# Optimization experiments

Measured on AMD Instinct MI355X. Metric: run time of the kernel, lower is better.

Reference implementation:

```python
import math
import jax, jax.numpy as jnp
import numpy as np

C = 256          # channels
HID = 64         # max(int(C*0.25),16)
RH = 64          # max(C//4,32) router hidden
N, S, H, W = 8, 64, 16, 16
LOW_FREQ_RATIO = 0.2
ROUTER_TEMP = 1.0
LN_EPS = 1e-5

def gelu(v):
    return jax.nn.gelu(v, approximate=False)

def bn1d(v, s, b):  # folded eval-mode BatchNorm1d: (N,C,S)
    return v * s[None, :, None] + b[None, :, None]

def conv1x1(v, w, b=None):  # v:(N,Cin,S), w:(Cout,Cin)
    o = jnp.einsum('oc,ncs->nos', w, v)
    if b is not None:
        o = o + b[None, :, None]
    return o

def convk(v, w):  # v:(N,Cin,S), w:(Cout,Cin,K), 'same' padding
    k = w.shape[-1]
    return jax.lax.conv_general_dilated(v, w, (1,), [(k // 2, k // 2)],
                                        dimension_numbers=('NCH', 'OIH', 'NCH'))

def setup_inputs():
    key = jax.random.key(0)
    ks = iter(jax.random.split(key, 64))
    def nrm(shape, sc=0.02):
        return jax.random.normal(next(ks), shape, jnp.float32) * sc
    d = {}
    d['x'] = jax.random.normal(next(ks), (N, C, S, H, W), jnp.float32)
    d['ln_g'] = jnp.ones((C,), jnp.float32)
    d['ln_b'] = jnp.zeros((C,), jnp.float32)
    for k in (3, 5, 7):
        d['mb_w%d' % k] = nrm((C, 3 * C, k))
        d['mb_s%d' % k] = 1.0 + nrm((C,))
        d['mb_b%d' % k] = nrm((C,))
    d['mf_w'] = nrm((C, C)); d['mf_s'] = 1.0 + nrm((C,)); d['mf_b'] = nrm((C,))
    d['pg_w1'] = nrm((HID, 3)); d['pg_s1'] = 1.0 + nrm((HID,)); d['pg_b1'] = nrm((HID,))
    d['pg_w2'] = nrm((C, HID)); d['pg_b2'] = nrm((C,))
    d['pp_w'] = nrm((C, C)); d['pp_s'] = 1.0 + nrm((C,)); d['pp_b'] = nrm((C,))
    d['mg_w'] = nrm((C, 2 * C)); d['mg_b'] = nrm((C,))
    d['mo_w1'] = nrm((C, 3 * C)); d['mo_s1'] = 1.0 + nrm((C,)); d['mo_b1'] = nrm((C,))
    d['mo_w2'] = nrm((C, C))
    d['rt_w1'] = nrm((RH, C + 5)); d['rt_b1'] = nrm((RH,))
    d['rt_w2'] = nrm((3, RH)); d['rt_b2'] = nrm((3,))
    d['bp_w1'] = nrm((C, 4 * C)); d['bp_s1'] = 1.0 + nrm((C,)); d['bp_b1'] = nrm((C,))
    d['bp_w2'] = nrm((C, C))
    d['res_scale'] = jnp.full((1, C, 1), 0.05, jnp.float32)
    d['fg_w'] = nrm((C, C)); d['fg_b'] = nrm((C,))
    d['sg_w'] = nrm((C, C)); d['sg_s'] = 1.0 + nrm((C,)); d['sg_b'] = nrm((C,))
    return d

def _forward(x, ln_g, ln_b, mb_w3, mb_s3, mb_b3, mb_w5, mb_s5, mb_b5,
             mb_w7, mb_s7, mb_b7, mf_w, mf_s, mf_b,
             pg_w1, pg_s1, pg_b1, pg_w2, pg_b2, pp_w, pp_s, pp_b,
             mg_w, mg_b, mo_w1, mo_s1, mo_b1, mo_w2,
             rt_w1, rt_b1, rt_w2, rt_b2, bp_w1, bp_s1, bp_b1, bp_w2,
             res_scale, fg_w, fg_b, sg_w, sg_s, sg_b):
    n, c, s = x.shape[:3]
    x32 = x.astype(jnp.float32)
    desc = x32.mean(axis=(-1, -2))                     # (N,C,S)
    t = desc.transpose(0, 2, 1)                        # (N,S,C)
    mu = t.mean(-1, keepdims=True)
    var = t.var(-1, keepdims=True)
    dn = (((t - mu) / jnp.sqrt(var + LN_EPS)) * ln_g + ln_b).transpose(0, 2, 1)  # (N,C,S)

    def tdiff(v, order):
        dd = v[:, :, order:] - v[:, :, :-order]
        return jnp.pad(dd, ((0, 0), (0, 0), (order, 0)))
    diff1 = tdiff(dn, 1)
    diff2 = tdiff(dn, 2)

    # motion branch (multi-kernel conv1d + BN + GELU)
    mi = jnp.concatenate([dn, diff1, diff2], axis=1)   # (N,3C,S)
    motion = 0.0
    for w, bs, bb in ((mb_w3, mb_s3, mb_b3), (mb_w5, mb_s5, mb_b5), (mb_w7, mb_s7, mb_b7)):
        motion = motion + gelu(bn1d(convk(mi, w), bs, bb))
    motion = gelu(bn1d(conv1x1(motion / 3.0, mf_w), mf_s, mf_b))

    # FFT-based cycle / phase estimation
    tokens = dn.transpose(0, 2, 1)                     # (N,S,C)
    freq = jnp.fft.rfft(tokens, axis=1, norm='ortho')  # (N,F,C) complex
    fe = jnp.abs(freq).mean(-1)                        # (N,F)
    Fb = fe.shape[1]
    low = min(max(int(round(Fb * LOW_FREQ_RATIO)), 1), Fb - 1)
    he = fe[:, low:]
    peak_rel = jnp.argmax(he, axis=-1)                 # (N,)
    peak_idx = peak_rel + low
    peak_val = jnp.take_along_axis(he, peak_rel[:, None], axis=1)
    cycle_conf = peak_val / jnp.maximum(he.sum(axis=1, keepdims=True), 1e-6)  # (N,1)
    peak_norm = peak_idx.astype(jnp.float32)[:, None] / float(Fb - 1)
    mean_freq = freq.mean(-1)                          # (N,F) complex
    dom = jnp.take_along_axis(mean_freq, peak_idx[:, None], axis=1)[:, 0]
    dom_phase = jnp.arctan2(dom.imag, dom.real)
    tax = jnp.arange(s, dtype=jnp.float32)
    ang = (2.0 * math.pi / max(s, 1)) * peak_idx.astype(jnp.float32)
    arg = ang[:, None] * tax[None, :] + dom_phase[:, None]
    phase_cos = jnp.cos(arg)[:, None, :]               # (N,1,S)
    phase_sin = jnp.sin(arg)[:, None, :]

    cycle_token = jnp.broadcast_to(cycle_conf[:, :, None], (n, 1, s))
    pf = jnp.concatenate([phase_cos, phase_sin, cycle_token], axis=1)  # (N,3,S)
    pgate = jax.nn.sigmoid(conv1x1(gelu(bn1d(conv1x1(pf, pg_w1), pg_s1, pg_b1)), pg_w2, pg_b2))
    phase = gelu(bn1d(conv1x1(dn * pgate, pp_w), pp_s, pp_b))

    # bidirectional EMA memory via lax.scan
    gate = jax.nn.sigmoid(conv1x1(jnp.concatenate([dn, jnp.abs(diff1)], axis=1), mg_w, mg_b))
    g = gate.transpose(2, 0, 1)                        # (S,N,C)
    dd = dn.transpose(2, 0, 1)
    def step(st, gd):
        gt, dt = gd
        st = gt * st + (1.0 - gt) * dt
        return st, st
    _, fo = jax.lax.scan(step, dd[0], (g[1:], dd[1:]))
    fwd_mem = jnp.concatenate([dd[:1], fo], axis=0).transpose(1, 2, 0)
    _, bo = jax.lax.scan(step, dd[-1], (g[-2::-1], dd[-2::-1]))
    bwd_mem = jnp.concatenate([dd[-1:], bo], axis=0)[::-1].transpose(1, 2, 0)
    memory = conv1x1(gelu(bn1d(conv1x1(
        jnp.concatenate([dn, fwd_mem, bwd_mem], axis=1), mo_w1), mo_s1, mo_b1)), mo_w2)

    # router
    seq_std = dn.std(axis=2).mean(axis=1, keepdims=True)
    diff_energy = jnp.abs(diff1).mean(axis=(1, 2))[:, None]
    motion_energy = jnp.abs(motion).mean(axis=(1, 2))[:, None]
    memory_energy = jnp.abs(memory - dn).mean(axis=(1, 2))[:, None]
    stats = jnp.concatenate([seq_std, diff_energy, cycle_conf, peak_norm,
                             memory_energy + motion_energy], axis=-1)
    ri = jnp.concatenate([dn.mean(-1), stats], axis=-1)  # (N,C+5)
    hdn = gelu(ri @ rt_w1.T + rt_b1)
    logits = hdn @ rt_w2.T + rt_b2
    bw = jax.nn.softmax(logits / max(ROUTER_TEMP, 1e-6), axis=-1)  # (N,3)
    fused = (bw[:, 0, None, None] * motion + bw[:, 1, None, None] * phase
             + bw[:, 2, None, None] * memory)

    delta = conv1x1(gelu(bn1d(conv1x1(
        jnp.concatenate([dn, fused, motion - phase, memory - dn], axis=1),
        bp_w1), bp_s1, bp_b1)), bp_w2)
    delta = delta * jax.nn.sigmoid(conv1x1(dn, fg_w, fg_b))
    delta = res_scale * delta
    delta = delta[:, :, :, None, None]                 # (N,C,S,1,1)

    sp = x32.mean(axis=2)                              # (N,C,H,W)
    sg_lin = jnp.einsum('oc,nchw->nohw', sg_w, sp)
    sgate = jax.nn.sigmoid(sg_lin * sg_s[None, :, None, None] + sg_b[None, :, None, None])
    delta = delta * sgate[:, :, None, :, :]            # (N,C,S,H,W)
    return x + delta.astype(x.dtype)

def reference(x, ln_g, ln_b, mb_w3, mb_s3, mb_b3, mb_w5, mb_s5, mb_b5,
              mb_w7, mb_s7, mb_b7, mf_w, mf_s, mf_b,
              pg_w1, pg_s1, pg_b1, pg_w2, pg_b2, pp_w, pp_s, pp_b,
              mg_w, mg_b, mo_w1, mo_s1, mo_b1, mo_w2,
              rt_w1, rt_b1, rt_w2, rt_b2, bp_w1, bp_s1, bp_b1, bp_w2,
              res_scale, fg_w, fg_b, sg_w, sg_s, sg_b):
    return _forward(x, ln_g, ln_b, mb_w3, mb_s3, mb_b3, mb_w5, mb_s5, mb_b5,
                    mb_w7, mb_s7, mb_b7, mf_w, mf_s, mf_b,
                    pg_w1, pg_s1, pg_b1, pg_w2, pg_b2, pp_w, pp_s, pp_b,
                    mg_w, mg_b, mo_w1, mo_s1, mo_b1, mo_w2,
                    rt_w1, rt_b1, rt_w2, rt_b2, bp_w1, bp_s1, bp_b1, bp_w2,
                    res_scale, fg_w, fg_b, sg_w, sg_s, sg_b)
```

## Files before the change

### kernel.cpp

```cpp
#include <hip/hip_runtime.h>
#include <math.h>

namespace {

constexpr int N_ = 8, C_ = 256, S_ = 64, HW_ = 256;
constexpr int NS = N_ * S_;
constexpr int NHW = N_ * HW_;

constexpr size_t O_DESC  = 0;
constexpr size_t O_DN    = 131072;
constexpr size_t O_MSUM  = 262144;
constexpr size_t O_MOT   = 393216;
constexpr size_t O_GATE  = 524288;
constexpr size_t O_HMO   = 655360;
constexpr size_t O_MEM   = 786432;
constexpr size_t O_PPIN  = 917504;
constexpr size_t O_PHASE = 1048576;
constexpr size_t O_FGATE = 1179648;
constexpr size_t O_HBP   = 1310720;
constexpr size_t O_DELTA = 1441792;
constexpr size_t O_GIB   = 1572864;
constexpr size_t O_MOI   = 1835008;
constexpr size_t O_BPI   = 2228224;
constexpr size_t O_SPT   = 2752512;
constexpr size_t O_SGATE = 3276800;
constexpr size_t O_FE    = 3801088;
constexpr size_t O_MFRE  = 3801600;
constexpr size_t O_MFIM  = 3802112;
constexpr size_t O_PK    = 3802624;
constexpr size_t O_BW    = 3802656;
constexpr size_t O_ATMF  = 3802688;
constexpr size_t O_ATMG  = 3868224;
constexpr size_t O_ATMO1 = 3999296;
constexpr size_t O_ATMO2 = 4195904;
constexpr size_t O_ATPP  = 4261440;
constexpr size_t O_ATBP1 = 4326976;
constexpr size_t O_ATBP2 = 4589120;
constexpr size_t O_ATFG  = 4654656;
constexpr size_t O_ATSG  = 4720192;
constexpr size_t O_WFRAG = 4785728;
constexpr size_t O_IM2   = 6850112;
constexpr size_t O_CONVC = 8226368;

typedef __attribute__((ext_vector_type(4))) float f32x4;
typedef __attribute__((ext_vector_type(8))) short s16x8;
typedef __attribute__((ext_vector_type(8))) unsigned short u16x8;

__device__ __forceinline__ float gelu_f(float v) {
  return 0.5f * v * (1.0f + erff(v * 0.70710678118654752f));
}
__device__ __forceinline__ float sigmoid_f(float v) {
  return 1.0f / (1.0f + expf(-v));
}
__device__ __forceinline__ unsigned short f2bf(float f) {
  unsigned int u = __float_as_uint(f);
  u += 0x7fffu + ((u >> 16) & 1u);
  return (unsigned short)(u >> 16);
}

__device__ __forceinline__ float block_sum256(float v, float* scratch) {
  #pragma unroll
  for (int off = 32; off; off >>= 1) v += __shfl_down(v, off, 64);
  int w = threadIdx.x >> 6;
  __syncthreads();
  if ((threadIdx.x & 63) == 0) scratch[w] = v;
  __syncthreads();
  return scratch[0] + scratch[1] + scratch[2] + scratch[3];
}

__global__ __launch_bounds__(256) void transpose_kernel(
    const float* __restrict__ wmf, const float* __restrict__ wmg,
    const float* __restrict__ wmo1, const float* __restrict__ wmo2,
    const float* __restrict__ wpp, const float* __restrict__ wbp1,
    const float* __restrict__ wbp2, const float* __restrict__ wfg,
    const float* __restrict__ wsg, float* __restrict__ ws) {
  __shared__ float tile[32][33];
  int xt = blockIdx.x, yt = blockIdx.y;
  const float* src; float* dst; int K;
  if      (xt < 8)   { src = wmf;  dst = ws + O_ATMF;  K = 256;  }
  else if (xt < 24)  { src = wmg;  dst = ws + O_ATMG;  K = 512;  xt -= 8;  }
  else if (xt < 48)  { src = wmo1; dst = ws + O_ATMO1; K = 768;  xt -= 24; }
  else if (xt < 56)  { src = wmo2; dst = ws + O_ATMO2; K = 256;  xt -= 48; }
  else if (xt < 64)  { src = wpp;  dst = ws + O_ATPP;  K = 256;  xt -= 56; }
  else if (xt < 96)  { src = wbp1; dst = ws + O_ATBP1; K = 1024; xt -= 64; }
  else if (xt < 104) { src = wbp2; dst = ws + O_ATBP2; K = 256;  xt -= 96; }
  else if (xt < 112) { src = wfg;  dst = ws + O_ATFG;  K = 256;  xt -= 104;}
  else               { src = wsg;  dst = ws + O_ATSG;  K = 256;  xt -= 112;}
  int tx = threadIdx.x & 31, ty = threadIdx.x >> 5;
  int c = xt * 32 + tx;
  #pragma unroll
  for (int i = 0; i < 4; ++i) {
    int r = yt * 32 + ty + i * 8;
    tile[ty + i * 8][tx] = src[(size_t)r * K + c];
  }
  __syncthreads();
  #pragma unroll
  for (int i = 0; i < 4; ++i) {
    int cc = xt * 32 + ty + i * 8;
    dst[(size_t)cc * 256 + yt * 32 + tx] = tile[tx][ty + i * 8];
  }
}

__global__ __launch_bounds__(256) void wfrag_kernel(
    const float* __restrict__ w3, const float* __restrict__ w5, const float* __restrict__ w7,
    unsigned short* __restrict__ wf) {
  int g = blockIdx.x * 256 + threadIdx.x;
  int lane = g & 63;
  int m16 = (g >> 6) % 48;
  int kchunk = (g >> 6) / 48;
  int o = m16 * 16 + (lane & 15);
  int conv = o >> 8, oc = o & 255;
  int q = lane >> 4;
  u16x8 out;
  #pragma unroll
  for (int j = 0; j < 8; ++j) {
    int k = kchunk * 32 + q * 8 + j;
    int ic = k / 7;
    int tau = k - ic * 7 - 3;
    float v = 0.f;
    if (conv == 0) {
      if (tau >= -1 && tau <= 1) v = w3[((size_t)oc * 768 + ic) * 3 + (tau + 1)];
    } else if (conv == 1) {
      if (tau >= -2 && tau <= 2) v = w5[((size_t)oc * 768 + ic) * 5 + (tau + 2)];
    } else {
      v = w7[((size_t)oc * 768 + ic) * 7 + (tau + 3)];
    }
    out[j] = f2bf(v);
  }
  *((u16x8*)wf + g) = out;
}

__global__ __launch_bounds__(256) void im2col_kernel(
    const float* __restrict__ dn_t, unsigned short* __restrict__ imf) {
  int g = blockIdx.x * 256 + threadIdx.x;
  int lane = g & 63;
  int c16 = (g >> 6) % 32;
  int kchunk = (g >> 6) / 32;
  int col = c16 * 16 + (lane & 15);
  int n = col >> 6, s = col & 63;
  int q = lane >> 4;
  const float* base = dn_t + (size_t)n * 16384;
  u16x8 out;
  #pragma unroll
  for (int j = 0; j < 8; ++j) {
    int k = kchunk * 32 + q * 8 + j;
    int ic = k / 7;
    int tau = k - ic * 7 - 3;
    int stream = ic >> 8, c = ic & 255;
    int sp = s + tau;
    float v = 0.f;
    if (sp >= 0 && sp < 64) {
      float d = base[(size_t)sp * 256 + c];
      if (stream == 0) v = d;
      else if (stream == 1) v = (sp >= 1) ? d - base[(size_t)(sp - 1) * 256 + c] : 0.f;
      else v = (sp >= 2) ? d - base[(size_t)(sp - 2) * 256 + c] : 0.f;
    }
    out[j] = f2bf(v);
  }
  *((u16x8*)imf + g) = out;
}

__global__ __launch_bounds__(256) void conv_mfma_kernel(
    const unsigned short* __restrict__ wf, const unsigned short* __restrict__ imf,
    float* __restrict__ partial) {
  int mt = blockIdx.x, nt = blockIdx.y, kp = blockIdx.z;
  int lane = threadIdx.x & 63;
  int w = threadIdx.x >> 6;
  int m16 = mt * 4 + w;
  const s16x8* wfp = (const s16x8*)wf;
  const s16x8* imp = (const s16x8*)imf;
  f32x4 acc0 = {0.f,0.f,0.f,0.f}, acc1 = {0.f,0.f,0.f,0.f};
  f32x4 acc2 = {0.f,0.f,0.f,0.f}, acc3 = {0.f,0.f,0.f,0.f};
  #pragma unroll 2
  for (int cc = 0; cc < 42; ++cc) {
    int kc = kp * 42 + cc;
    s16x8 a = wfp[(size_t)(kc * 48 + m16) * 64 + lane];
    s16x8 b0 = imp[(size_t)(kc * 32 + nt * 4 + 0) * 64 + lane];
    s16x8 b1 = imp[(size_t)(kc * 32 + nt * 4 + 1) * 64 + lane];
    s16x8 b2 = imp[(size_t)(kc * 32 + nt * 4 + 2) * 64 + lane];
    s16x8 b3 = imp[(size_t)(kc * 32 + nt * 4 + 3) * 64 + lane];
    acc0 = __builtin_amdgcn_mfma_f32_16x16x32_bf16(a, b0, acc0, 0, 0, 0);
    acc1 = __builtin_amdgcn_mfma_f32_16x16x32_bf16(a, b1, acc1, 0, 0, 0);
    acc2 = __builtin_amdgcn_mfma_f32_16x16x32_bf16(a, b2, acc2, 0, 0, 0);
    acc3 = __builtin_amdgcn_mfma_f32_16x16x32_bf16(a, b3, acc3, 0, 0, 0);
  }
  int q = lane >> 4, ln = lane & 15;
  int o0 = m16 * 16 + q * 4;
  float* pb = partial + (size_t)kp * 393216;
  #pragma unroll
  for (int r = 0; r < 4; ++r) {
    size_t row = (size_t)(o0 + r) * 512;
    pb[row + (nt * 4 + 0) * 16 + ln] = acc0[r];
    pb[row + (nt * 4 + 1) * 16 + ln] = acc1[r];
    pb[row + (nt * 4 + 2) * 16 + ln] = acc2[r];
    pb[row + (nt * 4 + 3) * 16 + ln] = acc3[r];
  }
}

__global__ __launch_bounds__(256) void combine_kernel(
    const float* __restrict__ P,
    const float* __restrict__ s3, const float* __restrict__ b3,
    const float* __restrict__ s5, const float* __restrict__ b5,
    const float* __restrict__ s7, const float* __restrict__ b7,
    float* __restrict__ msum) {
  __shared__ float tile[32][33];
  int col0 = blockIdx.x * 32, o0 = blockIdx.y * 32;
  int t = threadIdx.x;
  int cl = t & 31, orow = t >> 5;
  #pragma unroll
  for (int p = 0; p < 4; ++p) {
    int ol = p * 8 + orow;
    int o = o0 + ol, col = col0 + cl;
    float v3 = 0.f, v5 = 0.f, v7 = 0.f;
    #pragma unroll
    for (int kpp = 0; kpp < 4; ++kpp) {
      size_t base = (size_t)kpp * 393216 + col;
      v3 += P[base + (size_t)o * 512];
      v5 += P[base + (size_t)(o + 256) * 512];
      v7 += P[base + (size_t)(o + 512) * 512];
    }
    float tot = gelu_f(v3 * s3[o] + b3[o]) + gelu_f(v5 * s5[o] + b5[o]) + gelu_f(v7 * s7[o] + b7[o]);
    tile[ol][cl] = tot * (1.f / 3.f);
  }
  __syncthreads();
  #pragma unroll
  for (int p = 0; p < 4; ++p) {
    int coll = p * 8 + orow;
    msum[(size_t)(col0 + coll) * 256 + o0 + cl] = tile[cl][coll];
  }
}

__global__ __launch_bounds__(256) void reduce_x_kernel(
    const float* __restrict__ x, float* __restrict__ desc_t, float* __restrict__ sp_t) {
  int nc = blockIdx.x; int n = nc >> 8; int c = nc & 255;
  int t = threadIdx.x; int w = t >> 6; int l = t & 63;
  const float4* x4 = (const float4*)x + (size_t)nc * 4096;
  float4 sa = {0.f, 0.f, 0.f, 0.f};
  for (int i = 0; i < 16; ++i) {
    int s = w * 16 + i;
    float4 v = x4[(size_t)s * 64 + l];
    sa.x += v.x; sa.y += v.y; sa.z += v.z; sa.w += v.w;
    float ds = v.x + v.y + v.z + v.w;
    #pragma unroll
    for (int off = 32; off; off >>= 1) ds += __shfl_down(ds, off, 64);
    if (l == 0) desc_t[((size_t)n * 64 + s) * 256 + c] = ds * (1.f / 256.f);
  }
  __shared__ float4 lsp[4][64];
  lsp[w][l] = sa;
  __syncthreads();
  if (t < 64) {
    float4 a = lsp[0][t], b = lsp[1][t], c2 = lsp[2][t], d = lsp[3][t];
    float4 tot;
    tot.x = a.x + b.x + c2.x + d.x; tot.y = a.y + b.y + c2.y + d.y;
    tot.z = a.z + b.z + c2.z + d.z; tot.w = a.w + b.w + c2.w + d.w;
    size_t base = ((size_t)n * 256 + t * 4) * 256 + c;
    sp_t[base]       = tot.x * (1.f / 64.f);
    sp_t[base + 256] = tot.y * (1.f / 64.f);
    sp_t[base + 512] = tot.z * (1.f / 64.f);
    sp_t[base + 768] = tot.w * (1.f / 64.f);
  }
}

__global__ __launch_bounds__(256) void ln_kernel(
    const float* __restrict__ desc_t, const float* __restrict__ g,
    const float* __restrict__ b, float* __restrict__ dn_t) {
  __shared__ float sc[4];
  int col = blockIdx.x; int t = threadIdx.x;
  float v = desc_t[(size_t)col * 256 + t];
  float s1 = block_sum256(v, sc);
  float s2 = block_sum256(v * v, sc);
  float mu = s1 * (1.f / 256.f);
  float var = s2 * (1.f / 256.f) - mu * mu;
  float r = rsqrtf(var + 1e-5f);
  dn_t[(size_t)col * 256 + t] = (v - mu) * r * g[t] + b[t];
}

__global__ __launch_bounds__(256) void prep_mi_kernel(
    const float* __restrict__ dn_t,
    float* __restrict__ gib, float* __restrict__ moi, float* __restrict__ bpi) {
  int col = blockIdx.x; int c = threadIdx.x;
  int s = col & 63;
  float d = dn_t[(size_t)col * 256 + c];
  float d1 = (s >= 1) ? d - dn_t[(size_t)(col - 1) * 256 + c] : 0.f;
  gib[(size_t)col * 512 + c] = d;
  gib[(size_t)col * 512 + 256 + c] = fabsf(d1);
  moi[(size_t)col * 768 + c] = d;
  bpi[(size_t)col * 1024 + c] = d;
}

__global__ __launch_bounds__(256) void fft_kernel(
    const float* __restrict__ dn_t, float* __restrict__ fe,
    float* __restrict__ mfre, float* __restrict__ mfim) {
  int b = blockIdx.x; int n = b / 33; int f = b % 33;
  int t = threadIdx.x;
  __shared__ float cs[64], sn[64];
  __shared__ float sc[4];
  if (t < 64) {
    int ft = (f * t) & 63;
    float ang = -6.283185307179586f * (float)ft * (1.f / 64.f);
    cs[t] = cosf(ang); sn[t] = sinf(ang);
  }
  __syncthreads();
  float re = 0.f, im = 0.f;
  const float* base = dn_t + (size_t)n * 16384 + t;
  for (int s = 0; s < 64; ++s) {
    float v = base[(size_t)s * 256];
    re += v * cs[s]; im += v * sn[s];
  }
  re *= 0.125f; im *= 0.125f;
  float mag = sqrtf(re * re + im * im);
  float sm = block_sum256(mag, sc);
  float sr = block_sum256(re, sc);
  float si = block_sum256(im, sc);
  if (t == 0) {
    fe[b]   = sm * (1.f / 256.f);
    mfre[b] = sr * (1.f / 256.f);
    mfim[b] = si * (1.f / 256.f);
  }
}

__global__ __launch_bounds__(64) void peak_kernel(
    const float* __restrict__ fe, const float* __restrict__ mfre,
    const float* __restrict__ mfim, float* __restrict__ pk) {
  int n = blockIdx.x; int t = threadIdx.x;
  float v = (t < 26) ? fe[n * 33 + 7 + t] : -1e30f;
  int idx = t;
  float hs = (t < 26) ? v : 0.f;
  #pragma unroll
  for (int off = 32; off; off >>= 1) {
    float ov = __shfl_down(v, off, 64);
    int   oi = __shfl_down(idx, off, 64);
    float oh = __shfl_down(hs, off, 64);
    hs += oh;
    if (ov > v || (ov == v && oi < idx)) { v = ov; idx = oi; }
  }
  if (t == 0) {
    int pi = idx + 7;
    float conf = v / fmaxf(hs, 1e-6f);
    float pnorm = (float)pi * (1.f / 32.f);
    float re = mfre[n * 33 + pi], im = mfim[n * 33 + pi];
    float dph = atan2f(im, re);
    float ang = (6.283185307179586f / 64.f) * (float)pi;
    pk[n * 4 + 0] = conf; pk[n * 4 + 1] = pnorm; pk[n * 4 + 2] = dph; pk[n * 4 + 3] = ang;
  }
}

template <int K, int EPI>
__global__ __launch_bounds__(256) void gemm_kernel(
    const float* __restrict__ At, const float* __restrict__ B, float* __restrict__ out,
    const float* __restrict__ sc, const float* __restrict__ bi,
    const float* __restrict__ fg, const float* __restrict__ rs) {
  int t = threadIdx.x;
  int o = blockIdx.x * 64 + (t & 63);
  int col = blockIdx.y * 4 + (t >> 6);
  const float* bp = B + (size_t)col * K;
  float4 a0 = {0.f,0.f,0.f,0.f};
  for (int kk = 0; kk < K; kk += 4) {
    float4 b0 = *(const float4*)(bp + kk);
    a0.x += At[(size_t)(kk + 0) * 256 + o] * b0.x;
    a0.y += At[(size_t)(kk + 1) * 256 + o] * b0.y;
    a0.z += At[(size_t)(kk + 2) * 256 + o] * b0.z;
    a0.w += At[(size_t)(kk + 3) * 256 + o] * b0.w;
  }
  float v0 = (a0.x + a0.y) + (a0.z + a0.w);
  if constexpr (EPI == 0) { v0 = gelu_f(v0 * sc[o] + bi[o]); }
  else if constexpr (EPI == 1) { v0 = sigmoid_f(v0 + bi[o]); }
  else if constexpr (EPI == 3) { v0 *= fg[(size_t)col * 256 + o] * rs[o]; }
  else if constexpr (EPI == 4) { v0 = sigmoid_f(v0 * sc[o] + bi[o]); }
  out[(size_t)col * 256 + o] = v0;
}

__global__ __launch_bounds__(256) void scan_kernel(
    const float* __restrict__ dn_t, const float* __restrict__ gate_t, float* __restrict__ moi) {
  int n = blockIdx.x, half = blockIdx.y;
  int t = threadIdx.x;
  __shared__ float ld[64 * 128];
  __shared__ float lg[64 * 128];
  const float* dsrc = dn_t + (size_t)n * 16384 + half * 128;
  const float* gsrc = gate_t + (size_t)n * 16384 + half * 128;
  for (int i = t; i < 8192; i += 256) {
    int s = i >> 7, j = i & 127;
    ld[i] = dsrc[(size_t)s * 256 + j];
    lg[i] = gsrc[(size_t)s * 256 + j];
  }
  __syncthreads();
  int cl = t & 127;
  int c = half * 128 + cl;
  size_t ob = (size_t)n * 64 * 768 + c;
  if (t < 128) {
    float st = ld[cl];
    moi[ob + 256] = st;
    for (int s = 1; s < 64; ++s) {
      float g = lg[s * 128 + cl], d = ld[s * 128 + cl];
      st = g * st + (1.f - g) * d;
      moi[ob + (size_t)s * 768 + 256] = st;
    }
  } else {
    float st = ld[63 * 128 + cl];
    moi[ob + (size_t)63 * 768 + 512] = st;
    for (int s = 62; s >= 0; --s) {
      float g = lg[s * 128 + cl], d = ld[s * 128 + cl];
      st = g * st + (1.f - g) * d;
      moi[ob + (size_t)s * 768 + 512] = st;
    }
  }
}

__global__ __launch_bounds__(256) void pgate_kernel(
    const float* __restrict__ dn_t, const float* __restrict__ pk,
    const float* __restrict__ pg_w1, const float* __restrict__ pg_s1, const float* __restrict__ pg_b1,
    const float* __restrict__ pg_w2, const float* __restrict__ pg_b2, float* __restrict__ ppin) {
  int col = blockIdx.x; int n = col >> 6; int s = col & 63;
  int t = threadIdx.x;
  __shared__ float h[64];
  float conf = pk[n * 4 + 0], dph = pk[n * 4 + 2], ang = pk[n * 4 + 3];
  float arg = ang * (float)s + dph;
  float pc = cosf(arg), ps = sinf(arg);
  if (t < 64) {
    float v = pg_w1[t * 3 + 0] * pc + pg_w1[t * 3 + 1] * ps + pg_w1[t * 3 + 2] * conf;
    v = v * pg_s1[t] + pg_b1[t];
    h[t] = gelu_f(v);
  }
  __syncthreads();
  float acc = pg_b2[t];
  const float* wrow = pg_w2 + t * 64;
  #pragma unroll 8
  for (int j = 0; j < 64; ++j) acc += wrow[j] * h[j];
  float pg = sigmoid_f(acc);
  ppin[(size_t)col * 256 + t] = dn_t[(size_t)col * 256 + t] * pg;
}

__global__ __launch_bounds__(256) void router_kernel(
    const float* __restrict__ dn_t, const float* __restrict__ motion_t,
    const float* __restrict__ memory_t, const float* __restrict__ pk,
    const float* __restrict__ rt_w1, const float* __restrict__ rt_b1,
    const float* __restrict__ rt_w2, const float* __restrict__ rt_b2,
    float* __restrict__ bw) {
  int n = blockIdx.x; int c = threadIdx.x;
  __shared__ float ri[261];
  __shared__ float h2[64];
  __shared__ float lg[3];
  __shared__ float sc[4];
  float sum = 0.f, sq = 0.f, ad1 = 0.f, amot = 0.f, amem = 0.f, prev = 0.f;
  for (int s = 0; s < 64; ++s) {
    size_t i = ((size_t)n * 64 + s) * 256 + c;
    float d = dn_t[i];
    sum += d; sq += d * d;
    if (s > 0) ad1 += fabsf(d - prev);
    prev = d;
    amot += fabsf(motion_t[i]);
    amem += fabsf(memory_t[i] - d);
  }
  float mean = sum * (1.f / 64.f);
  float var = sq * (1.f / 64.f) - mean * mean;
  float stdc = sqrtf(fmaxf(var, 0.f));
  ri[c] = mean;
  float rstd = block_sum256(stdc, sc);
  float rad1 = block_sum256(ad1, sc);
  float rmot = block_sum256(amot, sc);
  float rmem = block_sum256(amem, sc);
  if (c == 0) {
    ri[256] = rstd * (1.f / 256.f);
    ri[257] = rad1 * (1.f / 16384.f);
    ri[258] = pk[n * 4 + 0];
    ri[259] = pk[n * 4 + 1];
    ri[260] = (rmem + rmot) * (1.f / 16384.f);
  }
  __syncthreads();
  if (c < 64) {
    float acc = rt_b1[c];
    const float* wrow = rt_w1 + c * 261;
    for (int i = 0; i < 261; ++i) acc += wrow[i] * ri[i];
    h2[c] = gelu_f(acc);
  }
  __syncthreads();
  if (c < 3) {
    float acc = rt_b2[c];
    const float* wrow = rt_w2 + c * 64;
    #pragma unroll 8
    for (int j = 0; j < 64; ++j) acc += wrow[j] * h2[j];
    lg[c] = acc;
  }
  __syncthreads();
  if (c == 0) {
    float m = fmaxf(lg[0], fmaxf(lg[1], lg[2]));
    float e0 = expf(lg[0] - m), e1 = expf(lg[1] - m), e2 = expf(lg[2] - m);
    float inv = 1.f / (e0 + e1 + e2);
    bw[n * 3 + 0] = e0 * inv; bw[n * 3 + 1] = e1 * inv; bw[n * 3 + 2] = e2 * inv;
  }
}

__global__ __launch_bounds__(256) void bp_prep_kernel(
    const float* __restrict__ motion_t, const float* __restrict__ phase_t,
    const float* __restrict__ memory_t, const float* __restrict__ dn_t,
    const float* __restrict__ bw, float* __restrict__ bpi) {
  int col = blockIdx.x; int c = threadIdx.x; int n = col >> 6;
  size_t i = (size_t)col * 256 + c;
  float m = motion_t[i], p = phase_t[i], me = memory_t[i], d = dn_t[i];
  float b0 = bw[n * 3 + 0], b1 = bw[n * 3 + 1], b2 = bw[n * 3 + 2];
  size_t base = (size_t)col * 1024;
  bpi[base + 256 + c] = b0 * m + b1 * p + b2 * me;
  bpi[base + 512 + c] = m - p;
  bpi[base + 768 + c] = me - d;
}

__global__ __launch_bounds__(256) void final_kernel(
    const float* __restrict__ x, const float* __restrict__ delta_t,
    const float* __restrict__ sgate_t, float* __restrict__ out) {
  int nc = blockIdx.x; int n = nc >> 8; int c = nc & 255;
  int t = threadIdx.x;
  __shared__ float dlt[64];
  __shared__ float4 sgs4[64];
  if (t < 64) dlt[t] = delta_t[((size_t)n * 64 + t) * 256 + c];
  ((float*)sgs4)[t] = sgate_t[((size_t)n * 256 + t) * 256 + c];
  __syncthreads();
  const float4* x4 = (const float4*)x + (size_t)nc * 4096;
  float4* o4 = (float4*)out + (size_t)nc * 4096;
  int w = t >> 6, l = t & 63;
  float4 sg = sgs4[l];
  for (int i = 0; i < 16; ++i) {
    int s = w * 16 + i;
    float d = dlt[s];
    float4 v = x4[(size_t)s * 64 + l];
    v.x += d * sg.x; v.y += d * sg.y; v.z += d * sg.z; v.w += d * sg.w;
    o4[(size_t)s * 64 + l] = v;
  }
}

}

extern "C" void kernel_launch(void* const* d_in, const int* in_sizes, int n_in,
                              void* d_out, int out_size, void* d_ws, size_t ws_size,
                              hipStream_t stream) {
  const float* x      = (const float*)d_in[0];
  const float* ln_g   = (const float*)d_in[1];
  const float* ln_b   = (const float*)d_in[2];
  const float* mb_w3  = (const float*)d_in[3];
  const float* mb_s3  = (const float*)d_in[4];
  const float* mb_b3  = (const float*)d_in[5];
  const float* mb_w5  = (const float*)d_in[6];
  const float* mb_s5  = (const float*)d_in[7];
  const float* mb_b5  = (const float*)d_in[8];
  const float* mb_w7  = (const float*)d_in[9];
  const float* mb_s7  = (const float*)d_in[10];
  const float* mb_b7  = (const float*)d_in[11];
  const float* mf_w   = (const float*)d_in[12];
  const float* mf_s   = (const float*)d_in[13];
  const float* mf_b   = (const float*)d_in[14];
  const float* pg_w1  = (const float*)d_in[15];
  const float* pg_s1  = (const float*)d_in[16];
  const float* pg_b1  = (const float*)d_in[17];
  const float* pg_w2  = (const float*)d_in[18];
  const float* pg_b2  = (const float*)d_in[19];
  const float* pp_w   = (const float*)d_in[20];
  const float* pp_s   = (const float*)d_in[21];
  const float* pp_b   = (const float*)d_in[22];
  const float* mg_w   = (const float*)d_in[23];
  const float* mg_b   = (const float*)d_in[24];
  const float* mo_w1  = (const float*)d_in[25];
  const float* mo_s1  = (const float*)d_in[26];
  const float* mo_b1  = (const float*)d_in[27];
  const float* mo_w2  = (const float*)d_in[28];
  const float* rt_w1  = (const float*)d_in[29];
  const float* rt_b1  = (const float*)d_in[30];
  const float* rt_w2  = (const float*)d_in[31];
  const float* rt_b2  = (const float*)d_in[32];
  const float* bp_w1  = (const float*)d_in[33];
  const float* bp_s1  = (const float*)d_in[34];
  const float* bp_b1  = (const float*)d_in[35];
  const float* bp_w2  = (const float*)d_in[36];
  const float* res_sc = (const float*)d_in[37];
  const float* fg_w   = (const float*)d_in[38];
  const float* fg_b   = (const float*)d_in[39];
  const float* sg_w   = (const float*)d_in[40];
  const float* sg_s   = (const float*)d_in[41];
  const float* sg_b   = (const float*)d_in[42];
  float* ws = (float*)d_ws;
  float* out = (float*)d_out;
  unsigned short* wfrag = (unsigned short*)(ws + O_WFRAG);
  unsigned short* im2   = (unsigned short*)(ws + O_IM2);

  transpose_kernel<<<dim3(120, 8), 256, 0, stream>>>(mf_w, mg_w, mo_w1, mo_w2,
      pp_w, bp_w1, bp_w2, fg_w, sg_w, ws);
  wfrag_kernel<<<2016, 256, 0, stream>>>(mb_w3, mb_w5, mb_w7, wfrag);
  reduce_x_kernel<<<2048, 256, 0, stream>>>(x, ws + O_DESC, ws + O_SPT);
  ln_kernel<<<512, 256, 0, stream>>>(ws + O_DESC, ln_g, ln_b, ws + O_DN);
  im2col_kernel<<<1344, 256, 0, stream>>>(ws + O_DN, im2);
  prep_mi_kernel<<<512, 256, 0, stream>>>(ws + O_DN, ws + O_GIB, ws + O_MOI, ws + O_BPI);
  fft_kernel<<<264, 256, 0, stream>>>(ws + O_DN, ws + O_FE, ws + O_MFRE, ws + O_MFIM);
  peak_kernel<<<8, 64, 0, stream>>>(ws + O_FE, ws + O_MFRE, ws + O_MFIM, ws + O_PK);
  conv_mfma_kernel<<<dim3(12, 8, 4), 256, 0, stream>>>(wfrag, im2, ws + O_CONVC);
  combine_kernel<<<dim3(16, 8), 256, 0, stream>>>(ws + O_CONVC, mb_s3, mb_b3, mb_s5, mb_b5, mb_s7, mb_b7, ws + O_MSUM);
  gemm_kernel<256, 0><<<dim3(4, 128), 256, 0, stream>>>(ws + O_ATMF, ws + O_MSUM, ws + O_MOT, mf_s, mf_b, nullptr, nullptr);
  gemm_kernel<512, 1><<<dim3(4, 128), 256, 0, stream>>>(ws + O_ATMG, ws + O_GIB, ws + O_GATE, nullptr, mg_b, nullptr, nullptr);
  scan_kernel<<<dim3(8, 2), 256, 0, stream>>>(ws + O_DN, ws + O_GATE, ws + O_MOI);
  gemm_kernel<768, 0><<<dim3(4, 128), 256, 0, stream>>>(ws + O_ATMO1, ws + O_MOI, ws + O_HMO, mo_s1, mo_b1, nullptr, nullptr);
  gemm_kernel<256, 2><<<dim3(4, 128), 256, 0, stream>>>(ws + O_ATMO2, ws + O_HMO, ws + O_MEM, nullptr, nullptr, nullptr, nullptr);
  pgate_kernel<<<512, 256, 0, stream>>>(ws + O_DN, ws + O_PK, pg_w1, pg_s1, pg_b1, pg_w2, pg_b2, ws + O_PPIN);
  gemm_kernel<256, 0><<<dim3(4, 128), 256, 0, stream>>>(ws + O_ATPP, ws + O_PPIN, ws + O_PHASE, pp_s, pp_b, nullptr, nullptr);
  gemm_kernel<256, 1><<<dim3(4, 128), 256, 0, stream>>>(ws + O_ATFG, ws + O_DN, ws + O_FGATE, nullptr, fg_b, nullptr, nullptr);
  router_kernel<<<8, 256, 0, stream>>>(ws + O_DN, ws + O_MOT, ws + O_MEM, ws + O_PK,
      rt_w1, rt_b1, rt_w2, rt_b2, ws + O_BW);
  bp_prep_kernel<<<512, 256, 0, stream>>>(ws + O_MOT, ws + O_PHASE, ws + O_MEM, ws + O_DN, ws + O_BW, ws + O_BPI);
  gemm_kernel<1024, 0><<<dim3(4, 128), 256, 0, stream>>>(ws + O_ATBP1, ws + O_BPI, ws + O_HBP, bp_s1, bp_b1, nullptr, nullptr);
  gemm_kernel<256, 3><<<dim3(4, 128), 256, 0, stream>>>(ws + O_ATBP2, ws + O_HBP, ws + O_DELTA, nullptr, nullptr, ws + O_FGATE, res_sc);
  gemm_kernel<256, 4><<<dim3(4, 512), 256, 0, stream>>>(ws + O_ATSG, ws + O_SPT, ws + O_SGATE, sg_s, sg_b, nullptr, nullptr);
  final_kernel<<<2048, 256, 0, stream>>>(x, ws + O_DELTA, ws + O_SGATE, out);
}
```

Baseline: 598.5 us.

## Fuse pipeline stages into per-column kernels to cut launches and intermediates

Merges the weight transpose and conv-weight fragment prep into one launch, and im2col plus the DFT feature pass into another. Chains of small GEMMs and their prep or epilogue steps become per-column fused kernels (gate, motion, memory, phase, delta) that stage inputs in shared memory. The peak-finding kernel is folded into its consumers. This removes many launches and global round trips of intermediates, but each fused kernel now does a 256-wide dot product per thread, streaming the weight matrices, over only 512 blocks, so parallelism per GEMM drops.

```diff
diff --git a/kernel.cpp b/kernel.cpp
--- a/kernel.cpp
+++ b/kernel.cpp
@@ -9,25 +9,17 @@
 
 constexpr size_t O_DESC  = 0;
 constexpr size_t O_DN    = 131072;
-constexpr size_t O_MSUM  = 262144;
 constexpr size_t O_MOT   = 393216;
 constexpr size_t O_GATE  = 524288;
-constexpr size_t O_HMO   = 655360;
 constexpr size_t O_MEM   = 786432;
-constexpr size_t O_PPIN  = 917504;
 constexpr size_t O_PHASE = 1048576;
-constexpr size_t O_FGATE = 1179648;
-constexpr size_t O_HBP   = 1310720;
 constexpr size_t O_DELTA = 1441792;
-constexpr size_t O_GIB   = 1572864;
-constexpr size_t O_MOI   = 1835008;
-constexpr size_t O_BPI   = 2228224;
+constexpr size_t O_SCN   = 1572864;
 constexpr size_t O_SPT   = 2752512;
 constexpr size_t O_SGATE = 3276800;
 constexpr size_t O_FE    = 3801088;
 constexpr size_t O_MFRE  = 3801600;
 constexpr size_t O_MFIM  = 3802112;
-constexpr size_t O_PK    = 3802624;
 constexpr size_t O_BW    = 3802656;
 constexpr size_t O_ATMF  = 3802688;
 constexpr size_t O_ATMG  = 3868224;
@@ -68,96 +60,213 @@
   return scratch[0] + scratch[1] + scratch[2] + scratch[3];
 }
 
-__global__ __launch_bounds__(256) void transpose_kernel(
+__device__ __forceinline__ void compute_pk(
+    int n, const float* __restrict__ fe, const float* __restrict__ mfre,
+    const float* __restrict__ mfim,
+    float& conf, float& pnorm, float& dph, float& ang) {
+  const float* f = fe + n * 33;
+  float best = f[7]; int bidx = 0; float hs = 0.f;
+  #pragma unroll
+  for (int i = 0; i < 26; ++i) {
+    float v = f[7 + i];
+    hs += v;
+    if (v > best) { best = v; bidx = i; }
+  }
+  int pi = bidx + 7;
+  conf = best / fmaxf(hs, 1e-6f);
+  pnorm = (float)pi * (1.f / 32.f);
+  dph = atan2f(mfim[n * 33 + pi], mfre[n * 33 + pi]);
+  ang = (6.283185307179586f / 64.f) * (float)pi;
+}
+
+__global__ __launch_bounds__(256) void weights_kernel(
     const float* __restrict__ wmf, const float* __restrict__ wmg,
     const float* __restrict__ wmo1, const float* __restrict__ wmo2,
     const float* __restrict__ wpp, const float* __restrict__ wbp1,
     const float* __restrict__ wbp2, const float* __restrict__ wfg,
-    const float* __restrict__ wsg, float* __restrict__ ws) {
-  __shared__ float tile[32][33];
-  int xt = blockIdx.x, yt = blockIdx.y;
-  const float* src; float* dst; int K;
-  if      (xt < 8)   { src = wmf;  dst = ws + O_ATMF;  K = 256;  }
-  else if (xt < 24)  { src = wmg;  dst = ws + O_ATMG;  K = 512;  xt -= 8;  }
-  else if (xt < 48)  { src = wmo1; dst = ws + O_ATMO1; K = 768;  xt -= 24; }
-  else if (xt < 56)  { src = wmo2; dst = ws + O_ATMO2; K = 256;  xt -= 48; }
-  else if (xt < 64)  { src = wpp;  dst = ws + O_ATPP;  K = 256;  xt -= 56; }
-  else if (xt < 96)  { src = wbp1; dst = ws + O_ATBP1; K = 1024; xt -= 64; }
-  else if (xt < 104) { src = wbp2; dst = ws + O_ATBP2; K = 256;  xt -= 96; }
-  else if (xt < 112) { src = wfg;  dst = ws + O_ATFG;  K = 256;  xt -= 104;}
-  else               { src = wsg;  dst = ws + O_ATSG;  K = 256;  xt -= 112;}
-  int tx = threadIdx.x & 31, ty = threadIdx.x >> 5;
-  int c = xt * 32 + tx;
-  #pragma unroll
-  for (int i = 0; i < 4; ++i) {
-    int r = yt * 32 + ty + i * 8;
-    tile[ty + i * 8][tx] = src[(size_t)r * K + c];
-  }
-  __syncthreads();
-  #pragma unroll
-  for (int i = 0; i < 4; ++i) {
-    int cc = xt * 32 + ty + i * 8;
-    dst[(size_t)cc * 256 + yt * 32 + tx] = tile[tx][ty + i * 8];
-  }
-}
-
-__global__ __launch_bounds__(256) void wfrag_kernel(
-    const float* __restrict__ w3, const float* __restrict__ w5, const float* __restrict__ w7,
-    unsigned short* __restrict__ wf) {
-  int g = blockIdx.x * 256 + threadIdx.x;
-  int lane = g & 63;
-  int m16 = (g >> 6) % 48;
-  int kchunk = (g >> 6) / 48;
-  int o = m16 * 16 + (lane & 15);
-  int conv = o >> 8, oc = o & 255;
-  int q = lane >> 4;
-  u16x8 out;
-  #pragma unroll
-  for (int j = 0; j < 8; ++j) {
-    int k = kchunk * 32 + q * 8 + j;
-    int ic = k / 7;
-    int tau = k - ic * 7 - 3;
-    float v = 0.f;
-    if (conv == 0) {
-      if (tau >= -1 && tau <= 1) v = w3[((size_t)oc * 768 + ic) * 3 + (tau + 1)];
-    } else if (conv == 1) {
-      if (tau >= -2 && tau <= 2) v = w5[((size_t)oc * 768 + ic) * 5 + (tau + 2)];
-    } else {
-      v = w7[((size_t)oc * 768 + ic) * 7 + (tau + 3)];
-    }
-    out[j] = f2bf(v);
-  }
-  *((u16x8*)wf + g) = out;
-}
-
-__global__ __launch_bounds__(256) void im2col_kernel(
-    const float* __restrict__ dn_t, unsigned short* __restrict__ imf) {
-  int g = blockIdx.x * 256 + threadIdx.x;
-  int lane = g & 63;
-  int c16 = (g >> 6) % 32;
-  int kchunk = (g >> 6) / 32;
-  int col = c16 * 16 + (lane & 15);
-  int n = col >> 6, s = col & 63;
-  int q = lane >> 4;
-  const float* base = dn_t + (size_t)n * 16384;
-  u16x8 out;
-  #pragma unroll
-  for (int j = 0; j < 8; ++j) {
-    int k = kchunk * 32 + q * 8 + j;
-    int ic = k / 7;
-    int tau = k - ic * 7 - 3;
-    int stream = ic >> 8, c = ic & 255;
-    int sp = s + tau;
-    float v = 0.f;
-    if (sp >= 0 && sp < 64) {
-      float d = base[(size_t)sp * 256 + c];
-      if (stream == 0) v = d;
-      else if (stream == 1) v = (sp >= 1) ? d - base[(size_t)(sp - 1) * 256 + c] : 0.f;
-      else v = (sp >= 2) ? d - base[(size_t)(sp - 2) * 256 + c] : 0.f;
-    }
-    out[j] = f2bf(v);
-  }
-  *((u16x8*)imf + g) = out;
+    const float* __restrict__ wsg, float* __restrict__ ws,
+    const float* __restrict__ w3, const float* __restrict__ w5,
+    const float* __restrict__ w7, unsigned short* __restrict__ wf) {
+  int bid = blockIdx.x;
+  if (bid < 960) {
+    __shared__ float tile[32][33];
+    int xt = bid % 120, yt = bid / 120;
+    const float* src; float* dst; int K;
+    if      (xt < 8)   { src = wmf;  dst = ws + O_ATMF;  K = 256;  }
+    else if (xt < 24)  { src = wmg;  dst = ws + O_ATMG;  K = 512;  xt -= 8;  }
+    else if (xt < 48)  { src = wmo1; dst = ws + O_ATMO1; K = 768;  xt -= 24; }
+    else if (xt < 56)  { src = wmo2; dst = ws + O_ATMO2; K = 256;  xt -= 48; }
+    else if (xt < 64)  { src = wpp;  dst = ws + O_ATPP;  K = 256;  xt -= 56; }
+    else if (xt < 96)  { src = wbp1; dst = ws + O_ATBP1; K = 1024; xt -= 64; }
+    else if (xt < 104) { src = wbp2; dst = ws + O_ATBP2; K = 256;  xt -= 96; }
+    else if (xt < 112) { src = wfg;  dst = ws + O_ATFG;  K = 256;  xt -= 104;}
+    else               { src = wsg;  dst = ws + O_ATSG;  K = 256;  xt -= 112;}
+    int tx = threadIdx.x & 31, ty = threadIdx.x >> 5;
+    int c = xt * 32 + tx;
+    #pragma unroll
+    for (int i = 0; i < 4; ++i) {
+      int r = yt * 32 + ty + i * 8;
+      tile[ty + i * 8][tx] = src[(size_t)r * K + c];
+    }
+    __syncthreads();
+    #pragma unroll
+    for (int i = 0; i < 4; ++i) {
+      int cc = xt * 32 + ty + i * 8;
+      dst[(size_t)cc * 256 + yt * 32 + tx] = tile[tx][ty + i * 8];
+    }
+  } else {
+    int g = (bid - 960) * 256 + threadIdx.x;
+    int lane = g & 63;
+    int m16 = (g >> 6) % 48;
+    int kchunk = (g >> 6) / 48;
+    int o = m16 * 16 + (lane & 15);
+    int conv = o >> 8, oc = o & 255;
+    int q = lane >> 4;
+    u16x8 outv;
+    #pragma unroll
+    for (int j = 0; j < 8; ++j) {
+      int k = kchunk * 32 + q * 8 + j;
+      int ic = k / 7;
+      int tau = k - ic * 7 - 3;
+      float v = 0.f;
+      if (conv == 0) {
+        if (tau >= -1 && tau <= 1) v = w3[((size_t)oc * 768 + ic) * 3 + (tau + 1)];
+      } else if (conv == 1) {
+        if (tau >= -2 && tau <= 2) v = w5[((size_t)oc * 768 + ic) * 5 + (tau + 2)];
+      } else {
+        v = w7[((size_t)oc * 768 + ic) * 7 + (tau + 3)];
+      }
+      outv[j] = f2bf(v);
+    }
+    *((u16x8*)wf + g) = outv;
+  }
+}
+
+__global__ __launch_bounds__(256) void reduce_x_kernel(
+    const float* __restrict__ x, float* __restrict__ desc_t, float* __restrict__ sp_t) {
+  int nc = blockIdx.x; int n = nc >> 8; int c = nc & 255;
+  int t = threadIdx.x; int w = t >> 6; int l = t & 63;
+  const float4* x4 = (const float4*)x + (size_t)nc * 4096;
+  float4 sa = {0.f, 0.f, 0.f, 0.f};
+  for (int i = 0; i < 16; ++i) {
+    int s = w * 16 + i;
+    float4 v = x4[(size_t)s * 64 + l];
+    sa.x += v.x; sa.y += v.y; sa.z += v.z; sa.w += v.w;
+    float ds = v.x + v.y + v.z + v.w;
+    #pragma unroll
+    for (int off = 32; off; off >>= 1) ds += __shfl_down(ds, off, 64);
+    if (l == 0) desc_t[((size_t)n * 64 + s) * 256 + c] = ds * (1.f / 256.f);
+  }
+  __shared__ float4 lsp[4][64];
+  lsp[w][l] = sa;
+  __syncthreads();
+  if (t < 64) {
+    float4 a = lsp[0][t], b = lsp[1][t], c2 = lsp[2][t], d = lsp[3][t];
+    float4 tot;
+    tot.x = a.x + b.x + c2.x + d.x; tot.y = a.y + b.y + c2.y + d.y;
+    tot.z = a.z + b.z + c2.z + d.z; tot.w = a.w + b.w + c2.w + d.w;
+    size_t base = ((size_t)n * 256 + t * 4) * 256 + c;
+    sp_t[base]       = tot.x * (1.f / 64.f);
+    sp_t[base + 256] = tot.y * (1.f / 64.f);
+    sp_t[base + 512] = tot.z * (1.f / 64.f);
+    sp_t[base + 768] = tot.w * (1.f / 64.f);
+  }
+}
+
+__global__ __launch_bounds__(256) void ln_kernel(
+    const float* __restrict__ desc_t, const float* __restrict__ g,
+    const float* __restrict__ b, float* __restrict__ dn_t) {
+  __shared__ float sc[4];
+  int col = blockIdx.x; int t = threadIdx.x;
+  float v = desc_t[(size_t)col * 256 + t];
+  float s1 = block_sum256(v, sc);
+  float s2 = block_sum256(v * v, sc);
+  float mu = s1 * (1.f / 256.f);
+  float var = s2 * (1.f / 256.f) - mu * mu;
+  float r = rsqrtf(var + 1e-5f);
+  dn_t[(size_t)col * 256 + t] = (v - mu) * r * g[t] + b[t];
+}
+
+__global__ __launch_bounds__(256) void gate_kernel(
+    const float* __restrict__ dn_t, const float* __restrict__ At_mg,
+    const float* __restrict__ mg_b, float* __restrict__ gate_t) {
+  __shared__ float gin[512];
+  int col = blockIdx.x; int t = threadIdx.x; int s = col & 63;
+  float d = dn_t[(size_t)col * 256 + t];
+  float d1 = (s >= 1) ? d - dn_t[(size_t)(col - 1) * 256 + t] : 0.f;
+  gin[t] = d;
+  gin[256 + t] = fabsf(d1);
+  __syncthreads();
+  float a0 = 0.f, a1 = 0.f, a2 = 0.f, a3 = 0.f;
+  #pragma unroll 4
+  for (int k = 0; k < 512; k += 4) {
+    a0 += At_mg[(size_t)(k + 0) * 256 + t] * gin[k + 0];
+    a1 += At_mg[(size_t)(k + 1) * 256 + t] * gin[k + 1];
+    a2 += At_mg[(size_t)(k + 2) * 256 + t] * gin[k + 2];
+    a3 += At_mg[(size_t)(k + 3) * 256 + t] * gin[k + 3];
+  }
+  gate_t[(size_t)col * 256 + t] = sigmoid_f(((a0 + a1) + (a2 + a3)) + mg_b[t]);
+}
+
+__global__ __launch_bounds__(256) void dnaux_kernel(
+    const float* __restrict__ dn_t, unsigned short* __restrict__ imf,
+    float* __restrict__ fe, float* __restrict__ mfre, float* __restrict__ mfim) {
+  int bid = blockIdx.x;
+  int t = threadIdx.x;
+  if (bid < 1344) {
+    int g = bid * 256 + t;
+    int lane = g & 63;
+    int c16 = (g >> 6) % 32;
+    int kchunk = (g >> 6) / 32;
+    int col = c16 * 16 + (lane & 15);
+    int n = col >> 6, s = col & 63;
+    int q = lane >> 4;
+    const float* base = dn_t + (size_t)n * 16384;
+    u16x8 outv;
+    #pragma unroll
+    for (int j = 0; j < 8; ++j) {
+      int k = kchunk * 32 + q * 8 + j;
+      int ic = k / 7;
+      int tau = k - ic * 7 - 3;
+      int stream = ic >> 8, c = ic & 255;
+      int sp = s + tau;
+      float v = 0.f;
+      if (sp >= 0 && sp < 64) {
+        float d = base[(size_t)sp * 256 + c];
+        if (stream == 0) v = d;
+        else if (stream == 1) v = (sp >= 1) ? d - base[(size_t)(sp - 1) * 256 + c] : 0.f;
+        else v = (sp >= 2) ? d - base[(size_t)(sp - 2) * 256 + c] : 0.f;
+      }
+      outv[j] = f2bf(v);
+    }
+    *((u16x8*)imf + g) = outv;
+  } else {
+    int b = bid - 1344; int n = b / 33; int f = b % 33;
+    __shared__ float cs[64], sn[64];
+    __shared__ float sc[4];
+    if (t < 64) {
+      int ft = (f * t) & 63;
+      float ang = -6.283185307179586f * (float)ft * (1.f / 64.f);
+      cs[t] = cosf(ang); sn[t] = sinf(ang);
+    }
+    __syncthreads();
+    float re = 0.f, im = 0.f;
+    const float* base = dn_t + (size_t)n * 16384 + t;
+    for (int s = 0; s < 64; ++s) {
+      float v = base[(size_t)s * 256];
+      re += v * cs[s]; im += v * sn[s];
+    }
+    re *= 0.125f; im *= 0.125f;
+    float mag = sqrtf(re * re + im * im);
+    float sm = block_sum256(mag, sc);
+    float sr = block_sum256(re, sc);
+    float si = block_sum256(im, sc);
+    if (t == 0) {
+      fe[b]   = sm * (1.f / 256.f);
+      mfre[b] = sr * (1.f / 256.f);
+      mfim[b] = si * (1.f / 256.f);
+    }
+  }
 }
 
 __global__ __launch_bounds__(256) void conv_mfma_kernel(
@@ -197,181 +306,39 @@
   }
 }
 
-__global__ __launch_bounds__(256) void combine_kernel(
+__global__ __launch_bounds__(256) void motion_kernel(
     const float* __restrict__ P,
     const float* __restrict__ s3, const float* __restrict__ b3,
     const float* __restrict__ s5, const float* __restrict__ b5,
     const float* __restrict__ s7, const float* __restrict__ b7,
-    float* __restrict__ msum) {
-  __shared__ float tile[32][33];
-  int col0 = blockIdx.x * 32, o0 = blockIdx.y * 32;
-  int t = threadIdx.x;
-  int cl = t & 31, orow = t >> 5;
+    const float* __restrict__ At_mf, const float* __restrict__ mf_s,
+    const float* __restrict__ mf_b, float* __restrict__ motion_t) {
+  __shared__ float ms[256];
+  int col = blockIdx.x; int t = threadIdx.x;
+  float v3 = 0.f, v5 = 0.f, v7 = 0.f;
   #pragma unroll
-  for (int p = 0; p < 4; ++p) {
-    int ol = p * 8 + orow;
-    int o = o0 + ol, col = col0 + cl;
-    float v3 = 0.f, v5 = 0.f, v7 = 0.f;
-    #pragma unroll
-    for (int kpp = 0; kpp < 4; ++kpp) {
-      size_t base = (size_t)kpp * 393216 + col;
-      v3 += P[base + (size_t)o * 512];
-      v5 += P[base + (size_t)(o + 256) * 512];
-      v7 += P[base + (size_t)(o + 512) * 512];
-    }
-    float tot = gelu_f(v3 * s3[o] + b3[o]) + gelu_f(v5 * s5[o] + b5[o]) + gelu_f(v7 * s7[o] + b7[o]);
-    tile[ol][cl] = tot * (1.f / 3.f);
-  }
-  __syncthreads();
-  #pragma unroll
-  for (int p = 0; p < 4; ++p) {
-    int coll = p * 8 + orow;
-    msum[(size_t)(col0 + coll) * 256 + o0 + cl] = tile[cl][coll];
-  }
-}
-
-__global__ __launch_bounds__(256) void reduce_x_kernel(
-    const float* __restrict__ x, float* __restrict__ desc_t, float* __restrict__ sp_t) {
-  int nc = blockIdx.x; int n = nc >> 8; int c = nc & 255;
-  int t = threadIdx.x; int w = t >> 6; int l = t & 63;
-  const float4* x4 = (const float4*)x + (size_t)nc * 4096;
-  float4 sa = {0.f, 0.f, 0.f, 0.f};
-  for (int i = 0; i < 16; ++i) {
-    int s = w * 16 + i;
-    float4 v = x4[(size_t)s * 64 + l];
-    sa.x += v.x; sa.y += v.y; sa.z += v.z; sa.w += v.w;
-    float ds = v.x + v.y + v.z + v.w;
-    #pragma unroll
-    for (int off = 32; off; off >>= 1) ds += __shfl_down(ds, off, 64);
-    if (l == 0) desc_t[((size_t)n * 64 + s) * 256 + c] = ds * (1.f / 256.f);
-  }
-  __shared__ float4 lsp[4][64];
-  lsp[w][l] = sa;
-  __syncthreads();
-  if (t < 64) {
-    float4 a = lsp[0][t], b = lsp[1][t], c2 = lsp[2][t], d = lsp[3][t];
-    float4 tot;
-    tot.x = a.x + b.x + c2.x + d.x; tot.y = a.y + b.y + c2.y + d.y;
-    tot.z = a.z + b.z + c2.z + d.z; tot.w = a.w + b.w + c2.w + d.w;
-    size_t base = ((size_t)n * 256 + t * 4) * 256 + c;
-    sp_t[base]       = tot.x * (1.f / 64.f);
-    sp_t[base + 256] = tot.y * (1.f / 64.f);
-    sp_t[base + 512] = tot.z * (1.f / 64.f);
-    sp_t[base + 768] = tot.w * (1.f / 64.f);
-  }
-}
-
-__global__ __launch_bounds__(256) void ln_kernel(
-    const float* __restrict__ desc_t, const float* __restrict__ g,
-    const float* __restrict__ b, float* __restrict__ dn_t) {
-  __shared__ float sc[4];
-  int col = blockIdx.x; int t = threadIdx.x;
-  float v = desc_t[(size_t)col * 256 + t];
-  float s1 = block_sum256(v, sc);
-  float s2 = block_sum256(v * v, sc);
-  float mu = s1 * (1.f / 256.f);
-  float var = s2 * (1.f / 256.f) - mu * mu;
-  float r = rsqrtf(var + 1e-5f);
-  dn_t[(size_t)col * 256 + t] = (v - mu) * r * g[t] + b[t];
-}
-
-__global__ __launch_bounds__(256) void prep_mi_kernel(
-    const float* __restrict__ dn_t,
-    float* __restrict__ gib, float* __restrict__ moi, float* __restrict__ bpi) {
-  int col = blockIdx.x; int c = threadIdx.x;
-  int s = col & 63;
-  float d = dn_t[(size_t)col * 256 + c];
-  float d1 = (s >= 1) ? d - dn_t[(size_t)(col - 1) * 256 + c] : 0.f;
-  gib[(size_t)col * 512 + c] = d;
-  gib[(size_t)col * 512 + 256 + c] = fabsf(d1);
-  moi[(size_t)col * 768 + c] = d;
-  bpi[(size_t)col * 1024 + c] = d;
-}
-
-__global__ __launch_bounds__(256) void fft_kernel(
-    const float* __restrict__ dn_t, float* __restrict__ fe,
-    float* __restrict__ mfre, float* __restrict__ mfim) {
-  int b = blockIdx.x; int n = b / 33; int f = b % 33;
-  int t = threadIdx.x;
-  __shared__ float cs[64], sn[64];
-  __shared__ float sc[4];
-  if (t < 64) {
-    int ft = (f * t) & 63;
-    float ang = -6.283185307179586f * (float)ft * (1.f / 64.f);
-    cs[t] = cosf(ang); sn[t] = sinf(ang);
-  }
-  __syncthreads();
-  float re = 0.f, im = 0.f;
-  const float* base = dn_t + (size_t)n * 16384 + t;
-  for (int s = 0; s < 64; ++s) {
-    float v = base[(size_t)s * 256];
-    re += v * cs[s]; im += v * sn[s];
-  }
-  re *= 0.125f; im *= 0.125f;
-  float mag = sqrtf(re * re + im * im);
-  float sm = block_sum256(mag, sc);
-  float sr = block_sum256(re, sc);
-  float si = block_sum256(im, sc);
-  if (t == 0) {
-    fe[b]   = sm * (1.f / 256.f);
-    mfre[b] = sr * (1.f / 256.f);
-    mfim[b] = si * (1.f / 256.f);
-  }
-}
-
-__global__ __launch_bounds__(64) void peak_kernel(
-    const float* __restrict__ fe, const float* __restrict__ mfre,
-    const float* __restrict__ mfim, float* __restrict__ pk) {
-  int n = blockIdx.x; int t = threadIdx.x;
-  float v = (t < 26) ? fe[n * 33 + 7 + t] : -1e30f;
-  int idx = t;
-  float hs = (t < 26) ? v : 0.f;
-  #pragma unroll
-  for (int off = 32; off; off >>= 1) {
-    float ov = __shfl_down(v, off, 64);
-    int   oi = __shfl_down(idx, off, 64);
-    float oh = __shfl_down(hs, off, 64);
-    hs += oh;
-    if (ov > v || (ov == v && oi < idx)) { v = ov; idx = oi; }
-  }
-  if (t == 0) {
-    int pi = idx + 7;
-    float conf = v / fmaxf(hs, 1e-6f);
-    float pnorm = (float)pi * (1.f / 32.f);
-    float re = mfre[n * 33 + pi], im = mfim[n * 33 + pi];
-    float dph = atan2f(im, re);
-    float ang = (6.283185307179586f / 64.f) * (float)pi;
-    pk[n * 4 + 0] = conf; pk[n * 4 + 1] = pnorm; pk[n * 4 + 2] = dph; pk[n * 4 + 3] = ang;
-  }
-}
-
-template <int K, int EPI>
-__global__ __launch_bounds__(256) void gemm_kernel(
-    const float* __restrict__ At, const float* __restrict__ B, float* __restrict__ out,
-    const float* __restrict__ sc, const float* __restrict__ bi,
-    const float* __restrict__ fg, const float* __restrict__ rs) {
-  int t = threadIdx.x;
-  int o = blockIdx.x * 64 + (t & 63);
-  int col = blockIdx.y * 4 + (t >> 6);
-  const float* bp = B + (size_t)col * K;
-  float4 a0 = {0.f,0.f,0.f,0.f};
-  for (int kk = 0; kk < K; kk += 4) {
-    float4 b0 = *(const float4*)(bp + kk);
-    a0.x += At[(size_t)(kk + 0) * 256 + o] * b0.x;
-    a0.y += At[(size_t)(kk + 1) * 256 + o] * b0.y;
-    a0.z += At[(size_t)(kk + 2) * 256 + o] * b0.z;
-    a0.w += At[(size_t)(kk + 3) * 256 + o] * b0.w;
-  }
-  float v0 = (a0.x + a0.y) + (a0.z + a0.w);
-  if constexpr (EPI == 0) { v0 = gelu_f(v0 * sc[o] + bi[o]); }
-  else if constexpr (EPI == 1) { v0 = sigmoid_f(v0 + bi[o]); }
-  else if constexpr (EPI == 3) { v0 *= fg[(size_t)col * 256 + o] * rs[o]; }
-  else if constexpr (EPI == 4) { v0 = sigmoid_f(v0 * sc[o] + bi[o]); }
-  out[(size_t)col * 256 + o] = v0;
+  for (int kp = 0; kp < 4; ++kp) {
+    size_t base = (size_t)kp * 393216 + col;
+    v3 += P[base + (size_t)t * 512];
+    v5 += P[base + (size_t)(t + 256) * 512];
+    v7 += P[base + (size_t)(t + 512) * 512];
+  }
+  float tot = gelu_f(v3 * s3[t] + b3[t]) + gelu_f(v5 * s5[t] + b5[t]) + gelu_f(v7 * s7[t] + b7[t]);
+  ms[t] = tot * (1.f / 3.f);
+  __syncthreads();
+  float a0 = 0.f, a1 = 0.f, a2 = 0.f, a3 = 0.f;
+  #pragma unroll 4
+  for (int k = 0; k < 256; k += 4) {
+    a0 += At_mf[(size_t)(k + 0) * 256 + t] * ms[k + 0];
+    a1 += At_mf[(size_t)(k + 1) * 256 + t] * ms[k + 1];
+    a2 += At_mf[(size_t)(k + 2) * 256 + t] * ms[k + 2];
+    a3 += At_mf[(size_t)(k + 3) * 256 + t] * ms[k + 3];
+  }
+  motion_t[(size_t)col * 256 + t] = gelu_f(((a0 + a1) + (a2 + a3)) * mf_s[t] + mf_b[t]);
 }
 
 __global__ __launch_bounds__(256) void scan_kernel(
-    const float* __restrict__ dn_t, const float* __restrict__ gate_t, float* __restrict__ moi) {
+    const float* __restrict__ dn_t, const float* __restrict__ gate_t, float* __restrict__ scn) {
   int n = blockIdx.x, half = blockIdx.y;
   int t = threadIdx.x;
   __shared__ float ld[64 * 128];
@@ -386,53 +353,100 @@
   __syncthreads();
   int cl = t & 127;
   int c = half * 128 + cl;
-  size_t ob = (size_t)n * 64 * 768 + c;
+  size_t ob = (size_t)n * 64 * 512 + c;
   if (t < 128) {
     float st = ld[cl];
-    moi[ob + 256] = st;
+    scn[ob] = st;
     for (int s = 1; s < 64; ++s) {
       float g = lg[s * 128 + cl], d = ld[s * 128 + cl];
       st = g * st + (1.f - g) * d;
-      moi[ob + (size_t)s * 768 + 256] = st;
+      scn[ob + (size_t)s * 512] = st;
     }
   } else {
     float st = ld[63 * 128 + cl];
-    moi[ob + (size_t)63 * 768 + 512] = st;
+    scn[ob + (size_t)63 * 512 + 256] = st;
     for (int s = 62; s >= 0; --s) {
       float g = lg[s * 128 + cl], d = ld[s * 128 + cl];
       st = g * st + (1.f - g) * d;
-      moi[ob + (size_t)s * 768 + 512] = st;
-    }
-  }
-}
-
-__global__ __launch_bounds__(256) void pgate_kernel(
-    const float* __restrict__ dn_t, const float* __restrict__ pk,
+      scn[ob + (size_t)s * 512 + 256] = st;
+    }
+  }
+}
+
+__global__ __launch_bounds__(256) void memory_kernel(
+    const float* __restrict__ dn_t, const float* __restrict__ scn,
+    const float* __restrict__ At1, const float* __restrict__ sc1, const float* __restrict__ bi1,
+    const float* __restrict__ At2, float* __restrict__ mem_t) {
+  __shared__ float bv[768];
+  __shared__ float h[256];
+  int col = blockIdx.x; int t = threadIdx.x;
+  bv[t]       = dn_t[(size_t)col * 256 + t];
+  bv[256 + t] = scn[(size_t)col * 512 + t];
+  bv[512 + t] = scn[(size_t)col * 512 + 256 + t];
+  __syncthreads();
+  float a0 = 0.f, a1 = 0.f, a2 = 0.f, a3 = 0.f;
+  #pragma unroll 4
+  for (int k = 0; k < 768; k += 4) {
+    a0 += At1[(size_t)(k + 0) * 256 + t] * bv[k + 0];
+    a1 += At1[(size_t)(k + 1) * 256 + t] * bv[k + 1];
+    a2 += At1[(size_t)(k + 2) * 256 + t] * bv[k + 2];
+    a3 += At1[(size_t)(k + 3) * 256 + t] * bv[k + 3];
+  }
+  h[t] = gelu_f(((a0 + a1) + (a2 + a3)) * sc1[t] + bi1[t]);
+  __syncthreads();
+  float c0 = 0.f, c1 = 0.f, c2 = 0.f, c3 = 0.f;
+  #pragma unroll 4
+  for (int k = 0; k < 256; k += 4) {
+    c0 += At2[(size_t)(k + 0) * 256 + t] * h[k + 0];
+    c1 += At2[(size_t)(k + 1) * 256 + t] * h[k + 1];
+    c2 += At2[(size_t)(k + 2) * 256 + t] * h[k + 2];
+    c3 += At2[(size_t)(k + 3) * 256 + t] * h[k + 3];
+  }
+  mem_t[(size_t)col * 256 + t] = (c0 + c1) + (c2 + c3);
+}
+
+__global__ __launch_bounds__(256) void phase_kernel(
+    const float* __restrict__ dn_t, const float* __restrict__ fe,
+    const float* __restrict__ mfre, const float* __restrict__ mfim,
     const float* __restrict__ pg_w1, const float* __restrict__ pg_s1, const float* __restrict__ pg_b1,
-    const float* __restrict__ pg_w2, const float* __restrict__ pg_b2, float* __restrict__ ppin) {
-  int col = blockIdx.x; int n = col >> 6; int s = col & 63;
-  int t = threadIdx.x;
-  __shared__ float h[64];
-  float conf = pk[n * 4 + 0], dph = pk[n * 4 + 2], ang = pk[n * 4 + 3];
+    const float* __restrict__ pg_w2, const float* __restrict__ pg_b2,
+    const float* __restrict__ At_pp, const float* __restrict__ pp_s, const float* __restrict__ pp_b,
+    float* __restrict__ phase_t) {
+  __shared__ float hh[64];
+  __shared__ float pin[256];
+  int col = blockIdx.x; int n = col >> 6; int s = col & 63; int t = threadIdx.x;
+  float conf, pnorm, dph, ang;
+  compute_pk(n, fe, mfre, mfim, conf, pnorm, dph, ang);
+  (void)pnorm;
   float arg = ang * (float)s + dph;
   float pc = cosf(arg), ps = sinf(arg);
   if (t < 64) {
     float v = pg_w1[t * 3 + 0] * pc + pg_w1[t * 3 + 1] * ps + pg_w1[t * 3 + 2] * conf;
-    v = v * pg_s1[t] + pg_b1[t];
-    h[t] = gelu_f(v);
+    hh[t] = gelu_f(v * pg_s1[t] + pg_b1[t]);
   }
   __syncthreads();
   float acc = pg_b2[t];
   const float* wrow = pg_w2 + t * 64;
   #pragma unroll 8
-  for (int j = 0; j < 64; ++j) acc += wrow[j] * h[j];
-  float pg = sigmoid_f(acc);
-  ppin[(size_t)col * 256 + t] = dn_t[(size_t)col * 256 + t] * pg;
+  for (int j = 0; j < 64; ++j) acc += wrow[j] * hh[j];
+  pin[t] = dn_t[(size_t)col * 256 + t] * sigmoid_f(acc);
+  __syncthreads();
+  float a0 = 0.f, a1 = 0.f, a2 = 0.f, a3 = 0.f;
+  #pragma unroll 4
+  for (int k = 0; k < 256; k += 4) {
+    a0 += At_pp[(size_t)(k + 0) * 256 + t] * pin[k + 0];
+    a1 += At_pp[(size_t)(k + 1) * 256 + t] * pin[k + 1];
+    a2 += At_pp[(size_t)(k + 2) * 256 + t] * pin[k + 2];
+    a3 += At_pp[(size_t)(k + 3) * 256 + t] * pin[k + 3];
+  }
+  phase_t[(size_t)col * 256 + t] = gelu_f(((a0 + a1) + (a2 + a3)) * pp_s[t] + pp_b[t]);
 }
 
 __global__ __launch_bounds__(256) void router_kernel(
     const float* __restrict__ dn_t, const float* __restrict__ motion_t,
-    const float* __restrict__ memory_t, const float* __restrict__ pk,
+    const float* __restrict__ memory_t,
+    const float* __restrict__ fe, const float* __restrict__ mfre,
+    const float* __restrict__ mfim,
     const float* __restrict__ rt_w1, const float* __restrict__ rt_b1,
     const float* __restrict__ rt_w2, const float* __restrict__ rt_b2,
     float* __restrict__ bw) {
@@ -460,10 +474,13 @@
   float rmot = block_sum256(amot, sc);
   float rmem = block_sum256(amem, sc);
   if (c == 0) {
+    float conf, pnorm, dph, ang;
+    compute_pk(n, fe, mfre, mfim, conf, pnorm, dph, ang);
+    (void)dph; (void)ang;
     ri[256] = rstd * (1.f / 256.f);
     ri[257] = rad1 * (1.f / 16384.f);
-    ri[258] = pk[n * 4 + 0];
-    ri[259] = pk[n * 4 + 1];
+    ri[258] = conf;
+    ri[259] = pnorm;
     ri[260] = (rmem + rmot) * (1.f / 16384.f);
   }
   __syncthreads();
@@ -490,18 +507,75 @@
   }
 }
 
-__global__ __launch_bounds__(256) void bp_prep_kernel(
-    const float* __restrict__ motion_t, const float* __restrict__ phase_t,
-    const float* __restrict__ memory_t, const float* __restrict__ dn_t,
-    const float* __restrict__ bw, float* __restrict__ bpi) {
-  int col = blockIdx.x; int c = threadIdx.x; int n = col >> 6;
-  size_t i = (size_t)col * 256 + c;
-  float m = motion_t[i], p = phase_t[i], me = memory_t[i], d = dn_t[i];
-  float b0 = bw[n * 3 + 0], b1 = bw[n * 3 + 1], b2 = bw[n * 3 + 2];
-  size_t base = (size_t)col * 1024;
-  bpi[base + 256 + c] = b0 * m + b1 * p + b2 * me;
-  bpi[base + 512 + c] = m - p;
-  bpi[base + 768 + c] = me - d;
+__global__ __launch_bounds__(256) void delta_kernel(
+    const float* __restrict__ dn_t, const float* __restrict__ motion_t,
+    const float* __restrict__ phase_t, const float* __restrict__ mem_t,
+    const float* __restrict__ bw,
+    const float* __restrict__ At_fg, const float* __restrict__ fg_b,
+    const float* __restrict__ At1, const float* __restrict__ sc1, const float* __restrict__ bi1,
+    const float* __restrict__ At2, const float* __restrict__ rs,
+    float* __restrict__ delta_t) {
+  __shared__ float bv[1024];
+  __shared__ float h[256];
+  int col = blockIdx.x; int n = col >> 6; int t = threadIdx.x;
+  size_t i = (size_t)col * 256 + t;
+  float d = dn_t[i], m = motion_t[i], p = phase_t[i], me = mem_t[i];
+  float w0 = bw[n * 3 + 0], w1 = bw[n * 3 + 1], w2 = bw[n * 3 + 2];
+  bv[t]       = d;
+  bv[256 + t] = w0 * m + w1 * p + w2 * me;
+  bv[512 + t] = m - p;
+  bv[768 + t] = me - d;
+  __syncthreads();
+  float f0 = 0.f, f1 = 0.f, f2 = 0.f, f3 = 0.f;
+  #pragma unroll 4
+  for (int k = 0; k < 256; k += 4) {
+    f0 += At_fg[(size_t)(k + 0) * 256 + t] * bv[k + 0];
+    f1 += At_fg[(size_t)(k + 1) * 256 + t] * bv[k + 1];
+    f2 += At_fg[(size_t)(k + 2) * 256 + t] * bv[k + 2];
+    f3 += At_fg[(size_t)(k + 3) * 256 + t] * bv[k + 3];
+  }
+  float fgv = sigmoid_f(((f0 + f1) + (f2 + f3)) + fg_b[t]);
+  float a0 = 0.f, a1 = 0.f, a2 = 0.f, a3 = 0.f;
+  #pragma unroll 4
+  for (int k = 0; k < 1024; k += 4) {
+    a0 += At1[(size_t)(k + 0) * 256 + t] * bv[k + 0];
+    a1 += At1[(size_t)(k + 1) * 256 + t] * bv[k + 1];
+    a2 += At1[(size_t)(k + 2) * 256 + t] * bv[k + 2];
+    a3 += At1[(size_t)(k + 3) * 256 + t] * bv[k + 3];
+  }
+  h[t] = gelu_f(((a0 + a1) + (a2 + a3)) * sc1[t] + bi1[t]);
+  __syncthreads();
+  float c0 = 0.f, c1 = 0.f, c2 = 0.f, c3 = 0.f;
+  #pragma unroll 4
+  for (int k = 0; k < 256; k += 4) {
+    c0 += At2[(size_t)(k + 0) * 256 + t] * h[k + 0];
+    c1 += At2[(size_t)(k + 1) * 256 + t] * h[k + 1];
+    c2 += At2[(size_t)(k + 2) * 256 + t] * h[k + 2];
+    c3 += At2[(size_t)(k + 3) * 256 + t] * h[k + 3];
+  }
+  delta_t[i] = ((c0 + c1) + (c2 + c3)) * fgv * rs[t];
+}
+
+template <int K, int EPI>
+__global__ __launch_bounds__(256) void gemm_kernel(
+    const float* __restrict__ At, const float* __restrict__ B, float* __restrict__ out,
+    const float* __restrict__ sc, const float* __restrict__ bi,
+    const float* __restrict__ fg, const float* __restrict__ rs) {
+  int t = threadIdx.x;
+  int o = blockIdx.x * 64 + (t & 63);
+  int col = blockIdx.y * 4 + (t >> 6);
+  const float* bp = B + (size_t)col * K;
+  float4 a0 = {0.f,0.f,0.f,0.f};
+  for (int kk = 0; kk < K; kk += 4) {
+    float4 b0 = *(const float4*)(bp + kk);
+    a0.x += At[(size_t)(kk + 0) * 256 + o] * b0.x;
+    a0.y += At[(size_t)(kk + 1) * 256 + o] * b0.y;
+    a0.z += At[(size_t)(kk + 2) * 256 + o] * b0.z;
+    a0.w += At[(size_t)(kk + 3) * 256 + o] * b0.w;
+  }
+  float v0 = (a0.x + a0.y) + (a0.z + a0.w);
+  if constexpr (EPI == 4) { v0 = sigmoid_f(v0 * sc[o] + bi[o]); }
+  out[(size_t)col * 256 + o] = v0;
 }
 
 __global__ __launch_bounds__(256) void final_kernel(
@@ -580,30 +654,26 @@
   unsigned short* wfrag = (unsigned short*)(ws + O_WFRAG);
   unsigned short* im2   = (unsigned short*)(ws + O_IM2);
 
-  transpose_kernel<<<dim3(120, 8), 256, 0, stream>>>(mf_w, mg_w, mo_w1, mo_w2,
-      pp_w, bp_w1, bp_w2, fg_w, sg_w, ws);
-  wfrag_kernel<<<2016, 256, 0, stream>>>(mb_w3, mb_w5, mb_w7, wfrag);
+  weights_kernel<<<2976, 256, 0, stream>>>(mf_w, mg_w, mo_w1, mo_w2, pp_w, bp_w1,
+      bp_w2, fg_w, sg_w, ws, mb_w3, mb_w5, mb_w7, wfrag);
   reduce_x_kernel<<<2048, 256, 0, stream>>>(x, ws + O_DESC, ws + O_SPT);
   ln_kernel<<<512, 256, 0, stream>>>(ws + O_DESC, ln_g, ln_b, ws + O_DN);
-  im2col_kernel<<<1344, 256, 0, stream>>>(ws + O_DN, im2);
-  prep_mi_kernel<<<512, 256, 0, stream>>>(ws + O_DN, ws + O_GIB, ws + O_MOI, ws + O_BPI);
-  fft_kernel<<<264, 256, 0, stream>>>(ws + O_DN, ws + O_FE, ws + O_MFRE, ws + O_MFIM);
-  peak_kernel<<<8, 64, 0, stream>>>(ws + O_FE, ws + O_MFRE, ws + O_MFIM, ws + O_PK);
+  gate_kernel<<<512, 256, 0, stream>>>(ws + O_DN, ws + O_ATMG, mg_b, ws + O_GATE);
+  dnaux_kernel<<<1608, 256, 0, stream>>>(ws + O_DN, im2, ws + O_FE, ws + O_MFRE, ws + O_MFIM);
   conv_mfma_kernel<<<dim3(12, 8, 4), 256, 0, stream>>>(wfrag, im2, ws + O_CONVC);
-  combine_kernel<<<dim3(16, 8), 256, 0, stream>>>(ws + O_CONVC, mb_s3, mb_b3, mb_s5, mb_b5, mb_s7, mb_b7, ws + O_MSUM);
-  gemm_kernel<256, 0><<<dim3(4, 128), 256, 0, stream>>>(ws + O_ATMF, ws + O_MSUM, ws + O_MOT, mf_s, mf_b, nullptr, nullptr);
-  gemm_kernel<512, 1><<<dim3(4, 128), 256, 0, stream>>>(ws + O_ATMG, ws + O_GIB, ws + O_GATE, nullptr, mg_b, nullptr, nullptr);
-  scan_kernel<<<dim3(8, 2), 256, 0, stream>>>(ws + O_DN, ws + O_GATE, ws + O_MOI);
-  gemm_kernel<768, 0><<<dim3(4, 128), 256, 0, stream>>>(ws + O_ATMO1, ws + O_MOI, ws + O_HMO, mo_s1, mo_b1, nullptr, nullptr);
-  gemm_kernel<256, 2><<<dim3(4, 128), 256, 0, stream>>>(ws + O_ATMO2, ws + O_HMO, ws + O_MEM, nullptr, nullptr, nullptr, nullptr);
-  pgate_kernel<<<512, 256, 0, stream>>>(ws + O_DN, ws + O_PK, pg_w1, pg_s1, pg_b1, pg_w2, pg_b2, ws + O_PPIN);
-  gemm_kernel<256, 0><<<dim3(4, 128), 256, 0, stream>>>(ws + O_ATPP, ws + O_PPIN, ws + O_PHASE, pp_s, pp_b, nullptr, nullptr);
-  gemm_kernel<256, 1><<<dim3(4, 128), 256, 0, stream>>>(ws + O_ATFG, ws + O_DN, ws + O_FGATE, nullptr, fg_b, nullptr, nullptr);
-  router_kernel<<<8, 256, 0, stream>>>(ws + O_DN, ws + O_MOT, ws + O_MEM, ws + O_PK,
-      rt_w1, rt_b1, rt_w2, rt_b2, ws + O_BW);
-  bp_prep_kernel<<<512, 256, 0, stream>>>(ws + O_MOT, ws + O_PHASE, ws + O_MEM, ws + O_DN, ws + O_BW, ws + O_BPI);
-  gemm_kernel<1024, 0><<<dim3(4, 128), 256, 0, stream>>>(ws + O_ATBP1, ws + O_BPI, ws + O_HBP, bp_s1, bp_b1, nullptr, nullptr);
-  gemm_kernel<256, 3><<<dim3(4, 128), 256, 0, stream>>>(ws + O_ATBP2, ws + O_HBP, ws + O_DELTA, nullptr, nullptr, ws + O_FGATE, res_sc);
-  gemm_kernel<256, 4><<<dim3(4, 512), 256, 0, stream>>>(ws + O_ATSG, ws + O_SPT, ws + O_SGATE, sg_s, sg_b, nullptr, nullptr);
+  motion_kernel<<<512, 256, 0, stream>>>(ws + O_CONVC, mb_s3, mb_b3, mb_s5, mb_b5,
+      mb_s7, mb_b7, ws + O_ATMF, mf_s, mf_b, ws + O_MOT);
+  scan_kernel<<<dim3(8, 2), 256, 0, stream>>>(ws + O_DN, ws + O_GATE, ws + O_SCN);
+  memory_kernel<<<512, 256, 0, stream>>>(ws + O_DN, ws + O_SCN, ws + O_ATMO1,
+      mo_s1, mo_b1, ws + O_ATMO2, ws + O_MEM);
+  phase_kernel<<<512, 256, 0, stream>>>(ws + O_DN, ws + O_FE, ws + O_MFRE, ws + O_MFIM,
+      pg_w1, pg_s1, pg_b1, pg_w2, pg_b2, ws + O_ATPP, pp_s, pp_b, ws + O_PHASE);
+  router_kernel<<<8, 256, 0, stream>>>(ws + O_DN, ws + O_MOT, ws + O_MEM,
+      ws + O_FE, ws + O_MFRE, ws + O_MFIM, rt_w1, rt_b1, rt_w2, rt_b2, ws + O_BW);
+  delta_kernel<<<512, 256, 0, stream>>>(ws + O_DN, ws + O_MOT, ws + O_PHASE, ws + O_MEM,
+      ws + O_BW, ws + O_ATFG, fg_b, ws + O_ATBP1, bp_s1, bp_b1, ws + O_ATBP2, res_sc,
+      ws + O_DELTA);
+  gemm_kernel<256, 4><<<dim3(4, 512), 256, 0, stream>>>(ws + O_ATSG, ws + O_SPT,
+      ws + O_SGATE, sg_s, sg_b, nullptr, nullptr);
   final_kernel<<<2048, 256, 0, stream>>>(x, ws + O_DELTA, ws + O_SGATE, out);
 }
```

Result: faster. 568.9 us (-4.9%).
